# Optimization experiments

Hardware: AMD Instinct MI355X
Metric: run time of the kernel (lower is better)

Reference implementation:

```python
import jax, jax.numpy as jnp
import numpy as np


def conv2d_same(x, w, b):
    # x: (B,C,H,W), w: (O,I,3,3) -> 3x3 'same' conv, stride 1
    y = jax.lax.conv_general_dilated(
        x, w, window_strides=(1, 1), padding=((1, 1), (1, 1)),
        dimension_numbers=("NCHW", "OIHW", "NCHW"))
    return y + b[None, :, None, None]


def setup_inputs() -> dict:
    key = jax.random.key(0)
    ks = jax.random.split(key, 7)
    B, F, E, H, W = 16, 64, 16, 64, 64
    fan2d = F * 9
    state = jax.random.normal(ks[0], (B, F, H, W), dtype=jnp.float32)
    pre_w = jax.random.normal(ks[1], (F, F, 3, 3), dtype=jnp.float32) / np.sqrt(fan2d)
    pre_b = jax.random.normal(ks[2], (F,), dtype=jnp.float32) * 0.01
    attn_w = jax.random.normal(ks[3], (E, F, 3, 3), dtype=jnp.float32) / np.sqrt(fan2d)
    attn_b = jax.random.normal(ks[4], (E,), dtype=jnp.float32) * 0.01
    c3_w = jax.random.normal(ks[5], (F, F), dtype=jnp.float32) / np.sqrt(F)
    c3_b = jax.random.normal(ks[6], (F,), dtype=jnp.float32) * 0.01
    return {"state": state, "pre_w": pre_w, "pre_b": pre_b,
            "attn_w": attn_w, "attn_b": attn_b, "c3_w": c3_w, "c3_b": c3_b}


def reference(state, pre_w, pre_b, attn_w, attn_b, c3_w, c3_b):
    # pre_conv + relu
    x = jax.nn.relu(conv2d_same(state, pre_w, pre_b))
    # visattn_conv + sigmoid -> (B,E,H,W)
    attn = jax.nn.sigmoid(conv2d_same(x, attn_w, attn_b))
    # einsum 'bfyx,beyx->bfeyx'
    x5 = state[:, :, None, :, :] * attn[:, None, :, :, :]  # (B,F,E,H,W)
    # Conv3d kernel (1,1,1) with padding (0,1,1): zero-pad H,W by 1,
    # then pointwise linear over F. Output spatial dims become (E, H+2, W+2).
    x5 = jnp.pad(x5, ((0, 0), (0, 0), (0, 0), (1, 1), (1, 1)))
    y = jnp.einsum("of,bfeyx->boeyx", c3_w, x5) + c3_b[None, :, None, None, None]
    y = jax.nn.relu(y)
    # permute (0,2,1,3,4) then mean over last two dims -> (B,E,F)
    out = jnp.mean(y, axis=(-1, -2)).transpose(0, 2, 1)
    return out, attn
```

## Files before the change

### kernel.cpp

```cpp
#include <hip/hip_runtime.h>
#include <math.h>

constexpr int B = 16, F = 64, E = 16, H = 64, W = 64;
constexpr int XP = 66;
constexpr int CP = 72;
constexpr int YSTRIDE = XP * F;

typedef __bf16 bf16x8 __attribute__((ext_vector_type(8)));
typedef __bf16 bf16x4 __attribute__((ext_vector_type(4)));
typedef float f32x16 __attribute__((ext_vector_type(16)));
typedef float f32x4 __attribute__((ext_vector_type(4)));

__global__ __launch_bounds__(256) void prep_kernel(
    const float* __restrict__ state, const float* __restrict__ pre_w,
    const float* __restrict__ attn_w, const float* __restrict__ c3_w,
    __bf16* __restrict__ xTs, __bf16* __restrict__ wA1,
    __bf16* __restrict__ wA2, __bf16* __restrict__ wT3b,
    float* __restrict__ out0)
{
    __shared__ float s_t[64][68];
    const int blk = blockIdx.x;
    const int tid = threadIdx.x;

    if (blk < 1024) {
        const int b = blk >> 6, y = blk & 63;
        {
            int c = tid >> 2, x0 = (tid & 3) * 16;
            const float* src = state + ((size_t)(b * F + c) * H + y) * W + x0;
            #pragma unroll
            for (int q = 0; q < 4; ++q)
                *(float4*)&s_t[c][x0 + 4 * q] = *(const float4*)(src + 4 * q);
        }
        __syncthreads();
        __bf16* dst = xTs + (size_t)(b * H + y) * YSTRIDE;
        #pragma unroll
        for (int i = 0; i < 2; ++i) {
            int t = tid + i * 256;
            int x = t >> 3, cg = t & 7;
            bf16x8 v;
            #pragma unroll
            for (int j = 0; j < 8; ++j) v[j] = (__bf16)s_t[cg * 8 + j][x];
            *(bf16x8*)(dst + (x + 1) * F + cg * 8) = v;
        }
        if (tid < 16) {
            int bd = tid >> 3, cg = tid & 7;
            bf16x8 z = {};
            *(bf16x8*)(dst + (bd ? 65 : 0) * F + cg * 8) = z;
        }
    } else if (blk < 1168) {
        int idx = (blk - 1024) * 256 + tid;
        if (idx < 64 * 576) {
            int o = idx / 576, rem = idx - o * 576, t = rem >> 6, c = rem & 63;
            wA1[idx] = (__bf16)pre_w[(o * 64 + c) * 9 + t];
        }
        if (idx < 16 * 576) {
            int e = idx / 576, rem = idx - e * 576, t = rem >> 6, c = rem & 63;
            wA2[idx] = (__bf16)attn_w[(e * 64 + c) * 9 + t];
        }
        if (idx < 64 * 64) {
            wT3b[idx] = (__bf16)c3_w[idx];
        }
    } else {
        int idx = (blk - 1168) * 256 + tid;
        float4 z = {0.f, 0.f, 0.f, 0.f};
        *(float4*)(out0 + idx * 4) = z;
    }
}

__global__ __launch_bounds__(256) void conv1_mfma(
    const __bf16* __restrict__ xTs, const __bf16* __restrict__ wA1,
    const float* __restrict__ bias, __bf16* __restrict__ xT1)
{
    __shared__ __bf16 s_x[4 * XP * CP];
    const int b = blockIdx.y, y0 = blockIdx.x * 2;
    const int tid = threadIdx.x;

    for (int t = tid; t < 4 * XP * 8; t += 256) {
        int r = t / (XP * 8);
        int rem = t - r * (XP * 8);
        int x = rem >> 3, cg = rem & 7;
        int yy = y0 - 1 + r;
        bf16x8 v = {};
        if (yy >= 0 && yy < H)
            v = *(const bf16x8*)(xTs + (size_t)(b * H + yy) * YSTRIDE + x * F + cg * 8);
        *(bf16x8*)(s_x + (r * XP + x) * CP + cg * 8) = v;
    }
    __syncthreads();

    const int wave = tid >> 6, lane = tid & 63;
    const int mt = wave & 1;
    const int np = wave >> 1;
    const int n = lane & 31, kh = lane >> 5;
    f32x16 acc0 = {}, acc1 = {};
    const __bf16* aBase = wA1 + (mt * 32 + n) * 576 + kh * 8;

    #pragma unroll
    for (int dy = 0; dy < 3; ++dy) {
        #pragma unroll
        for (int dx = 0; dx < 3; ++dx) {
            const int t9 = dy * 3 + dx;
            const __bf16* bBase = s_x + ((np + dy) * XP + (n + dx)) * CP + kh * 8;
            #pragma unroll
            for (int cq = 0; cq < 4; ++cq) {
                bf16x8 a  = *(const bf16x8*)(aBase + t9 * 64 + cq * 16);
                bf16x8 b0 = *(const bf16x8*)(bBase + cq * 16);
                bf16x8 b1 = *(const bf16x8*)(bBase + 32 * CP + cq * 16);
                acc0 = __builtin_amdgcn_mfma_f32_32x32x16_bf16(a, b0, acc0, 0, 0, 0);
                acc1 = __builtin_amdgcn_mfma_f32_32x32x16_bf16(a, b1, acc1, 0, 0, 0);
            }
        }
    }

    __bf16* obase = xT1 + (size_t)(b * H + y0 + np) * YSTRIDE;
    #pragma unroll
    for (int g = 0; g < 4; ++g) {
        int o0 = mt * 32 + kh * 4 + g * 8;
        f32x4 b4 = *(const f32x4*)(bias + o0);
        bf16x4 v0, v1;
        #pragma unroll
        for (int r = 0; r < 4; ++r) {
            v0[r] = (__bf16)fmaxf(acc0[g * 4 + r] + b4[r], 0.f);
            v1[r] = (__bf16)fmaxf(acc1[g * 4 + r] + b4[r], 0.f);
        }
        *(bf16x4*)(obase + (n + 1) * F + o0) = v0;
        *(bf16x4*)(obase + (n + 33) * F + o0) = v1;
    }
    if (tid < 32) {
        int r2 = tid >> 4, bd = (tid >> 3) & 1, cg = tid & 7;
        bf16x8 z = {};
        *(bf16x8*)(xT1 + (size_t)(b * H + y0 + r2) * YSTRIDE + (bd ? 65 : 0) * F + cg * 8) = z;
    }
}

__global__ __launch_bounds__(256) void conv2_reduce(
    const __bf16* __restrict__ xT1, const __bf16* __restrict__ xTs,
    const __bf16* __restrict__ wA2, const __bf16* __restrict__ wT3b,
    const float* __restrict__ attn_b, const float* __restrict__ c3_b,
    float* __restrict__ attn_out, float* __restrict__ out)
{
    __shared__ __align__(16) char smem[38912];
    const int b = blockIdx.y, yp = blockIdx.x;
    const int tid = threadIdx.x;
    const int wave = tid >> 6, lane = tid & 63;
    const int y0 = yp * 2;

    __bf16* sx = (__bf16*)smem;
    float (*s_attn)[64][16] = (float(*)[64][16])smem;
    float (*s_sp)[68] = (float(*)[68])(smem + 8192);

    for (int t = tid; t < 4 * XP * 8; t += 256) {
        int r = t / (XP * 8), rem = t - r * (XP * 8);
        int x = rem >> 3, cg = rem & 7;
        int yy = y0 - 1 + r;
        bf16x8 v = {};
        if (yy >= 0 && yy < H)
            v = *(const bf16x8*)(xT1 + (size_t)(b * H + yy) * YSTRIDE + x * F + cg * 8);
        *(bf16x8*)(sx + (r * XP + x) * CP + cg * 8) = v;
    }
    __syncthreads();

    const int rw = wave >> 1, nt2 = wave & 1;
    const int n16 = lane & 15, quad = lane >> 4;
    f32x4 acc2[2] = {};
    {
        const __bf16* aB = wA2 + n16 * 576 + quad * 8;
        #pragma unroll
        for (int dy = 0; dy < 3; ++dy)
            #pragma unroll
            for (int dx = 0; dx < 3; ++dx) {
                const int t9 = dy * 3 + dx;
                #pragma unroll
                for (int cq = 0; cq < 2; ++cq) {
                    bf16x8 a = *(const bf16x8*)(aB + t9 * 64 + cq * 32);
                    #pragma unroll
                    for (int i = 0; i < 2; ++i) {
                        const __bf16* bp = sx +
                            ((rw + dy) * XP + (nt2 * 32 + i * 16 + n16 + dx)) * CP
                            + quad * 8 + cq * 32;
                        acc2[i] = __builtin_amdgcn_mfma_f32_16x16x32_bf16(
                            a, *(const bf16x8*)bp, acc2[i], 0, 0, 0);
                    }
                }
            }
    }
    __syncthreads();

    #pragma unroll
    for (int i = 0; i < 2; ++i) {
        int x = nt2 * 32 + i * 16 + n16;
        #pragma unroll
        for (int r = 0; r < 4; ++r) {
            int e = quad * 4 + r;
            float val = acc2[i][r] + attn_b[e];
            float sg = 1.f / (1.f + __expf(-val));
            attn_out[((size_t)(b * E + e) * H + (y0 + rw)) * W + x] = sg;
            s_attn[rw][x][e] = sg;
        }
    }
    __syncthreads();

    const int combo = tid & 63;
    const int eg = combo >> 4, og = combo & 15, psub = tid >> 6;
    f32x4 cb4 = ((const f32x4*)c3_b)[og];
    float vsum[4] = {0.f, 0.f, 0.f, 0.f};

    for (int rr = 0; rr < 2; ++rr) {
        {
            const int mt = wave & 1, nt = wave >> 1;
            const int n = lane & 31, kh = lane >> 5;
            const __bf16* bBase = xTs + (size_t)(b * H + y0 + rr) * YSTRIDE
                                  + (nt * 32 + n + 1) * F + kh * 8;
            const __bf16* aBase = wT3b + (mt * 32 + n) * 64 + kh * 8;
            f32x16 acc = {};
            #pragma unroll
            for (int cq = 0; cq < 4; ++cq) {
                bf16x8 a  = *(const bf16x8*)(aBase + cq * 16);
                bf16x8 bb = *(const bf16x8*)(bBase + cq * 16);
                acc = __builtin_amdgcn_mfma_f32_32x32x16_bf16(a, bb, acc, 0, 0, 0);
            }
            #pragma unroll
            for (int g = 0; g < 4; ++g)
                #pragma unroll
                for (int r = 0; r < 4; ++r)
                    s_sp[nt * 32 + n][mt * 32 + kh * 4 + g * 8 + r] = acc[g * 4 + r];
        }
        __syncthreads();

        float accl[4][4] = {};
        #pragma unroll 2
        for (int pp = 0; pp < 16; ++pp) {
            int p = psub * 16 + pp;
            f32x4 a4 = *(const f32x4*)&s_attn[rr][p][eg * 4];
            f32x4 s4 = *(const f32x4*)&s_sp[p][og * 4];
            #pragma unroll
            for (int i = 0; i < 4; ++i)
                #pragma unroll
                for (int j = 0; j < 4; ++j)
                    accl[i][j] += fmaxf(fmaf(a4[i], s4[j], cb4[j]), 0.f);
        }
        __syncthreads();
        float* s_part = &s_sp[0][0];
        #pragma unroll
        for (int i = 0; i < 4; ++i)
            #pragma unroll
            for (int j = 0; j < 4; ++j)
                s_part[(psub * 64 + combo) * 16 + i * 4 + j] = accl[i][j];
        __syncthreads();
        {
            int cmb = tid >> 2, ii = tid & 3;
            #pragma unroll
            for (int j = 0; j < 4; ++j) {
                float v = 0.f;
                #pragma unroll
                for (int ps = 0; ps < 4; ++ps)
                    v += s_part[(ps * 64 + cmb) * 16 + ii * 4 + j];
                vsum[j] += v;
            }
        }
        __syncthreads();
    }
    {
        int cmb = tid >> 2, ii = tid & 3;
        int e = (cmb >> 4) * 4 + ii;
        #pragma unroll
        for (int j = 0; j < 4; ++j) {
            int o = (cmb & 15) * 4 + j;
            float add = vsum[j] * (1.f / 4356.f);
            if (yp == 0) add += 260.f * fmaxf(c3_b[o], 0.f) * (1.f / 4356.f);
            atomicAdd(&out[(b * E + e) * F + o], add);
        }
    }
}

extern "C" void kernel_launch(void* const* d_in, const int* in_sizes, int n_in,
                              void* d_out, int out_size, void* d_ws, size_t ws_size,
                              hipStream_t stream) {
    (void)in_sizes; (void)n_in; (void)out_size; (void)ws_size;
    const float* state  = (const float*)d_in[0];
    const float* pre_w  = (const float*)d_in[1];
    const float* pre_b  = (const float*)d_in[2];
    const float* attn_w = (const float*)d_in[3];
    const float* attn_b = (const float*)d_in[4];
    const float* c3_w   = (const float*)d_in[5];
    const float* c3_b   = (const float*)d_in[6];

    float* out      = (float*)d_out;
    float* attn_out = out + B * E * F;

    char* ws = (char*)d_ws;
    constexpr size_t XT_BYTES = (size_t)B * H * YSTRIDE * 2;
    __bf16* xTs  = (__bf16*)ws;
    __bf16* xT1  = (__bf16*)(ws + XT_BYTES);
    __bf16* wA1  = (__bf16*)(ws + 2 * XT_BYTES);
    __bf16* wA2  = (__bf16*)(ws + 2 * XT_BYTES + 73728);
    __bf16* wT3b = (__bf16*)(ws + 2 * XT_BYTES + 73728 + 18432);

    prep_kernel<<<1184, 256, 0, stream>>>(state, pre_w, attn_w, c3_w,
                                          xTs, wA1, wA2, wT3b, out);
    conv1_mfma<<<dim3(H / 2, B), 256, 0, stream>>>(xTs, wA1, pre_b, xT1);
    conv2_reduce<<<dim3(H / 2, B), 256, 0, stream>>>(xT1, xTs, wA2, wT3b,
                                                     attn_b, c3_b, attn_out, out);
}
```

Measured before the change: 116.4 us.

## Fuse conv1 into conv2 kernel with halo recompute in shared memory

Merges the first 3x3 conv (pre_conv+relu) into the attention/reduce kernel. Each block recomputes the four conv1 output rows it needs, one per wave, writing them straight into shared memory, so the intermediate xT1 buffer in global memory and one kernel launch go away. In exchange conv1 work doubles because of halo recompute (4 rows computed per 2 output rows). The conv1 operands are now read directly from global/L2 rather than staged in LDS, and the per-wave compute is larger.

```diff
diff --git a/kernel.cpp b/kernel.cpp
--- a/kernel.cpp
+++ b/kernel.cpp
@@ -67,95 +67,84 @@
     }
 }
 
-__global__ __launch_bounds__(256) void conv1_mfma(
+__global__ __launch_bounds__(256) void mega_kernel(
     const __bf16* __restrict__ xTs, const __bf16* __restrict__ wA1,
-    const float* __restrict__ bias, __bf16* __restrict__ xT1)
-{
-    __shared__ __bf16 s_x[4 * XP * CP];
-    const int b = blockIdx.y, y0 = blockIdx.x * 2;
-    const int tid = threadIdx.x;
-
-    for (int t = tid; t < 4 * XP * 8; t += 256) {
-        int r = t / (XP * 8);
-        int rem = t - r * (XP * 8);
-        int x = rem >> 3, cg = rem & 7;
-        int yy = y0 - 1 + r;
-        bf16x8 v = {};
-        if (yy >= 0 && yy < H)
-            v = *(const bf16x8*)(xTs + (size_t)(b * H + yy) * YSTRIDE + x * F + cg * 8);
-        *(bf16x8*)(s_x + (r * XP + x) * CP + cg * 8) = v;
-    }
-    __syncthreads();
-
-    const int wave = tid >> 6, lane = tid & 63;
-    const int mt = wave & 1;
-    const int np = wave >> 1;
-    const int n = lane & 31, kh = lane >> 5;
-    f32x16 acc0 = {}, acc1 = {};
-    const __bf16* aBase = wA1 + (mt * 32 + n) * 576 + kh * 8;
-
-    #pragma unroll
-    for (int dy = 0; dy < 3; ++dy) {
-        #pragma unroll
-        for (int dx = 0; dx < 3; ++dx) {
-            const int t9 = dy * 3 + dx;
-            const __bf16* bBase = s_x + ((np + dy) * XP + (n + dx)) * CP + kh * 8;
-            #pragma unroll
-            for (int cq = 0; cq < 4; ++cq) {
-                bf16x8 a  = *(const bf16x8*)(aBase + t9 * 64 + cq * 16);
-                bf16x8 b0 = *(const bf16x8*)(bBase + cq * 16);
-                bf16x8 b1 = *(const bf16x8*)(bBase + 32 * CP + cq * 16);
-                acc0 = __builtin_amdgcn_mfma_f32_32x32x16_bf16(a, b0, acc0, 0, 0, 0);
-                acc1 = __builtin_amdgcn_mfma_f32_32x32x16_bf16(a, b1, acc1, 0, 0, 0);
-            }
-        }
-    }
-
-    __bf16* obase = xT1 + (size_t)(b * H + y0 + np) * YSTRIDE;
-    #pragma unroll
-    for (int g = 0; g < 4; ++g) {
-        int o0 = mt * 32 + kh * 4 + g * 8;
-        f32x4 b4 = *(const f32x4*)(bias + o0);
-        bf16x4 v0, v1;
-        #pragma unroll
-        for (int r = 0; r < 4; ++r) {
-            v0[r] = (__bf16)fmaxf(acc0[g * 4 + r] + b4[r], 0.f);
-            v1[r] = (__bf16)fmaxf(acc1[g * 4 + r] + b4[r], 0.f);
-        }
-        *(bf16x4*)(obase + (n + 1) * F + o0) = v0;
-        *(bf16x4*)(obase + (n + 33) * F + o0) = v1;
-    }
-    if (tid < 32) {
-        int r2 = tid >> 4, bd = (tid >> 3) & 1, cg = tid & 7;
-        bf16x8 z = {};
-        *(bf16x8*)(xT1 + (size_t)(b * H + y0 + r2) * YSTRIDE + (bd ? 65 : 0) * F + cg * 8) = z;
-    }
-}
-
-__global__ __launch_bounds__(256) void conv2_reduce(
-    const __bf16* __restrict__ xT1, const __bf16* __restrict__ xTs,
     const __bf16* __restrict__ wA2, const __bf16* __restrict__ wT3b,
-    const float* __restrict__ attn_b, const float* __restrict__ c3_b,
+    const float* __restrict__ pre_b, const float* __restrict__ attn_b,
+    const float* __restrict__ c3_b,
     float* __restrict__ attn_out, float* __restrict__ out)
 {
-    __shared__ __align__(16) char smem[38912];
+    __shared__ __align__(16) char smem[4 * XP * CP * 2];
     const int b = blockIdx.y, yp = blockIdx.x;
     const int tid = threadIdx.x;
     const int wave = tid >> 6, lane = tid & 63;
     const int y0 = yp * 2;
 
-    __bf16* sx = (__bf16*)smem;
+    __bf16* sxo = (__bf16*)smem;
     float (*s_attn)[64][16] = (float(*)[64][16])smem;
     float (*s_sp)[68] = (float(*)[68])(smem + 8192);
 
-    for (int t = tid; t < 4 * XP * 8; t += 256) {
-        int r = t / (XP * 8), rem = t - r * (XP * 8);
-        int x = rem >> 3, cg = rem & 7;
-        int yy = y0 - 1 + r;
-        bf16x8 v = {};
-        if (yy >= 0 && yy < H)
-            v = *(const bf16x8*)(xT1 + (size_t)(b * H + yy) * YSTRIDE + x * F + cg * 8);
-        *(bf16x8*)(sx + (r * XP + x) * CP + cg * 8) = v;
+    {
+        const int n = lane & 31, kh = lane >> 5;
+        const int yr = y0 - 1 + wave;
+        f32x16 acc[4] = {};
+        if (yr >= 0 && yr < H) {
+            #pragma unroll
+            for (int dy = 0; dy < 3; ++dy) {
+                const int row = yr - 1 + dy;
+                if (row >= 0 && row < H) {
+                    const __bf16* rbase = xTs + (size_t)(b * H + row) * YSTRIDE;
+                    #pragma unroll
+                    for (int dx = 0; dx < 3; ++dx) {
+                        const int t9 = dy * 3 + dx;
+                        #pragma unroll
+                        for (int cq = 0; cq < 4; ++cq) {
+                            const int ko = cq * 16 + kh * 8;
+                            bf16x8 a0 = *(const bf16x8*)(wA1 + n * 576 + t9 * 64 + ko);
+                            bf16x8 a1 = *(const bf16x8*)(wA1 + (32 + n) * 576 + t9 * 64 + ko);
+                            bf16x8 b0 = *(const bf16x8*)(rbase + (n + dx) * F + ko);
+                            bf16x8 b1 = *(const bf16x8*)(rbase + (n + dx + 32) * F + ko);
+                            acc[0] = __builtin_amdgcn_mfma_f32_32x32x16_bf16(a0, b0, acc[0], 0, 0, 0);
+                            acc[1] = __builtin_amdgcn_mfma_f32_32x32x16_bf16(a0, b1, acc[1], 0, 0, 0);
+                            acc[2] = __builtin_amdgcn_mfma_f32_32x32x16_bf16(a1, b0, acc[2], 0, 0, 0);
+                            acc[3] = __builtin_amdgcn_mfma_f32_32x32x16_bf16(a1, b1, acc[3], 0, 0, 0);
+                        }
+                    }
+                }
+            }
+            __bf16* orow = sxo + wave * XP * CP;
+            #pragma unroll
+            for (int mt = 0; mt < 2; ++mt)
+                #pragma unroll
+                for (int g = 0; g < 4; ++g) {
+                    int o0 = mt * 32 + kh * 4 + g * 8;
+                    f32x4 b4 = *(const f32x4*)(pre_b + o0);
+                    bf16x4 v0, v1;
+                    #pragma unroll
+                    for (int r = 0; r < 4; ++r) {
+                        v0[r] = (__bf16)fmaxf(acc[mt * 2 + 0][g * 4 + r] + b4[r], 0.f);
+                        v1[r] = (__bf16)fmaxf(acc[mt * 2 + 1][g * 4 + r] + b4[r], 0.f);
+                    }
+                    *(bf16x4*)(orow + (n + 1) * CP + o0) = v0;
+                    *(bf16x4*)(orow + (n + 33) * CP + o0) = v1;
+                }
+        } else {
+            __bf16* orow = sxo + wave * XP * CP;
+            bf16x4 z = {};
+            #pragma unroll
+            for (int mt = 0; mt < 2; ++mt)
+                #pragma unroll
+                for (int g = 0; g < 4; ++g) {
+                    int o0 = mt * 32 + kh * 4 + g * 8;
+                    *(bf16x4*)(orow + (n + 1) * CP + o0) = z;
+                    *(bf16x4*)(orow + (n + 33) * CP + o0) = z;
+                }
+        }
+        if (tid < 64) {
+            int r = tid >> 4, bd = (tid >> 3) & 1, cg = tid & 7;
+            bf16x8 z = {};
+            *(bf16x8*)(sxo + (r * XP + (bd ? 65 : 0)) * CP + cg * 8) = z;
+        }
     }
     __syncthreads();
 
@@ -174,7 +163,7 @@
                     bf16x8 a = *(const bf16x8*)(aB + t9 * 64 + cq * 32);
                     #pragma unroll
                     for (int i = 0; i < 2; ++i) {
-                        const __bf16* bp = sx +
+                        const __bf16* bp = sxo +
                             ((rw + dy) * XP + (nt2 * 32 + i * 16 + n16 + dx)) * CP
                             + quad * 8 + cq * 32;
                         acc2[i] = __builtin_amdgcn_mfma_f32_16x16x32_bf16(
@@ -290,14 +279,13 @@
     char* ws = (char*)d_ws;
     constexpr size_t XT_BYTES = (size_t)B * H * YSTRIDE * 2;
     __bf16* xTs  = (__bf16*)ws;
-    __bf16* xT1  = (__bf16*)(ws + XT_BYTES);
-    __bf16* wA1  = (__bf16*)(ws + 2 * XT_BYTES);
-    __bf16* wA2  = (__bf16*)(ws + 2 * XT_BYTES + 73728);
-    __bf16* wT3b = (__bf16*)(ws + 2 * XT_BYTES + 73728 + 18432);
+    __bf16* wA1  = (__bf16*)(ws + XT_BYTES);
+    __bf16* wA2  = (__bf16*)(ws + XT_BYTES + 73728);
+    __bf16* wT3b = (__bf16*)(ws + XT_BYTES + 73728 + 18432);
 
     prep_kernel<<<1184, 256, 0, stream>>>(state, pre_w, attn_w, c3_w,
                                           xTs, wA1, wA2, wT3b, out);
-    conv1_mfma<<<dim3(H / 2, B), 256, 0, stream>>>(xTs, wA1, pre_b, xT1);
-    conv2_reduce<<<dim3(H / 2, B), 256, 0, stream>>>(xT1, xTs, wA2, wT3b,
-                                                     attn_b, c3_b, attn_out, out);
+    mega_kernel<<<dim3(H / 2, B), 256, 0, stream>>>(xTs, wA1, wA2, wT3b,
+                                                    pre_b, attn_b, c3_b,
+                                                    attn_out, out);
 }
```

Result: slower. 130.1 us (+11.7%).
